# Performance work log

Measured on AMD Instinct MI355X. Metric: run time of the kernel, lower is better.

Reference implementation:

```python
import jax, jax.numpy as jnp
import numpy as np

DIMS = 3; B = 256; N = 256; K = 16; HID = 64; INC = 64; F = 64; EPG = 8192; DEPTH = 3
EPS = 1e-15


def setup_inputs() -> dict:
    key = jax.random.key(0)
    ks = jax.random.split(key, 16)
    E = B * EPG
    g = jnp.repeat(jnp.arange(B), EPG)
    row = (g * N + jax.random.randint(ks[0], (E,), 0, N)).astype(jnp.int32)
    col = (g * N + jax.random.randint(ks[1], (E,), 0, N)).astype(jnp.int32)
    edge_index = jnp.stack([row, col])
    edge_attr = jax.random.uniform(ks[2], (E, DIMS), dtype=jnp.float32)
    x = jax.random.normal(ks[3], (B * N, INC), dtype=jnp.float32)
    x_to_pool = jax.random.normal(ks[4], (B * N, F * DIMS), dtype=jnp.float32)
    batch = jnp.repeat(jnp.arange(B), N).astype(jnp.int32)
    def w(k, shape, fan):
        return (jax.random.normal(k, shape, dtype=jnp.float32) / np.float32(np.sqrt(fan)))
    return dict(
        x=x, edge_attr=edge_attr, x_to_pool=x_to_pool,
        Wm0=w(ks[5], (DIMS, INC, HID), INC), Ws0=w(ks[6], (DIMS, INC, HID), INC), b0=jnp.zeros((DIMS, HID), jnp.float32),
        Wm1=w(ks[7], (DIMS, HID, HID), HID), Ws1=w(ks[8], (DIMS, HID, HID), HID), b1=jnp.zeros((DIMS, HID), jnp.float32),
        Wm2=w(ks[9], (DIMS, HID, K), HID), Ws2=w(ks[10], (DIMS, HID, K), HID), b2=jnp.zeros((DIMS, K), jnp.float32),
        fcW1=w(ks[11], (HID * (DEPTH - 1) + K, 50), HID * (DEPTH - 1) + K), fcb1=jnp.zeros((50,), jnp.float32),
        fcW2=w(ks[12], (50, K), 50), fcb2=jnp.zeros((K,), jnp.float32),
        edge_index=edge_index, batch=batch,
    )


def reference(x, edge_attr, x_to_pool, Wm0, Ws0, b0, Wm1, Ws1, b1, Wm2, Ws2, b2,
              fcW1, fcb1, fcW2, fcb2, edge_index, batch):
    row, col = edge_index[0], edge_index[1]
    n_total = B * N

    # ---- batch_to_adj: scatter edge list into dense (dims, B, N, N) adjacency ----
    ge, rl, cl = row // N, row % N, col % N
    adj = jnp.zeros((DIMS, B, N, N), x.dtype).at[:, ge, rl, cl].add(edge_attr.T)

    # ---- ParallelResGraphConv: per-dim edge-weighted graph conv stack ----
    def gconv(h, we, Wm, Ws, b):
        agg = jax.ops.segment_sum(we[:, None] * h[col], row, num_segments=n_total)
        return jax.nn.relu(agg @ Wm + h @ Ws + b)

    assignments = []
    for d in range(DIMS):  # small fixed loop over parallel streams
        we = edge_attr[:, d]
        h0 = gconv(x, we, Wm0[d], Ws0[d], b0[d])
        h1 = gconv(h0, we, Wm1[d], Ws1[d], b1[d])
        h2 = gconv(h1, we, Wm2[d], Ws2[d], b2[d])
        conv_out = jnp.concatenate([h0, h1, h2], axis=-1)  # [BN, HID*2+K]
        logits = (conv_out @ fcW1 + fcb1) @ fcW2 + fcb2     # shared pool_fc
        assignments.append(logits)
    s = jax.nn.softmax(jnp.stack(assignments).reshape(DIMS, B, N, K), axis=-1)

    # ---- losses: modularity (edge gather) + entropy ----
    a_flat = s.reshape(DIMS, n_total, K)
    mod = jnp.float32(0.0)
    for d in range(DIMS):
        diff = a_flat[d, row] - a_flat[d, col]
        mod = mod + jnp.mean(edge_attr[:, d] * jnp.sum(diff * diff, axis=-1))
    ent = jnp.mean(jnp.sum(-s * jnp.log(s + EPS), axis=-1))
    loss = mod + ent

    # ---- DiffPool-style pooling ----
    xr = x_to_pool.reshape(n_total, F, DIMS)
    xr = jnp.transpose(xr, (2, 0, 1)).reshape(DIMS, B, N, F)
    px = jnp.einsum('dbnk,dbnf->dbkf', s, xr)
    tmp = jnp.einsum('dbnk,dbnm->dbkm', s, adj)
    padj = jnp.einsum('dbkm,dbml->dbkl', tmp, s)
    scale = jnp.float32(K / N)
    px = jnp.transpose(px, (1, 2, 3, 0)).reshape(B * K, F, DIMS) * scale
    padj = padj * (scale * scale)

    # ---- adj_to_tg_batch: dense pooled adjacency back to edge list (fixed shapes) ----
    rows = jnp.repeat(jnp.arange(K), K)
    cols = jnp.tile(jnp.arange(K), K)
    off = (jnp.arange(B) * K)[:, None]
    pei = jnp.stack([(off + rows[None, :]).reshape(-1), (off + cols[None, :]).reshape(-1)]).astype(jnp.int32)
    pea = jax.lax.stop_gradient(jnp.transpose(padj, (1, 2, 3, 0)).reshape(-1, DIMS))  # detach_pool=True
    pbatch = jnp.repeat(jnp.arange(B), K).astype(jnp.int32)
    return (px, pei, pea, pbatch, loss, s)
```

## Files before the change

### kernel.cpp

```cpp
#include <hip/hip_runtime.h>

#define DIMS 3
#define NB 256
#define NN 256
#define KK 16
#define HID 64
#define EPG 8192
#define NTOT (NB*NN)
#define NE (NB*EPG)

#define PX_OFF   0
#define PEI_OFF  786432
#define PEA_OFF  917504
#define PB_OFF   1114112
#define LOSS_OFF 1118208
#define S_OFF    1118209

#define WREC_WS  0
#define CLREC_WS 25165824
#define IPTR_WS  27262976
#define ENT_WS   27526144
#define MOD_WS   27529216
#define WC_WS    27532288
#define BC_WS    27541504

__global__ void fc_combine(const float* __restrict__ fcW1, const float* __restrict__ fcb1,
                           const float* __restrict__ fcW2, const float* __restrict__ fcb2,
                           float* __restrict__ wc, float* __restrict__ bc)
{
    const int t = threadIdx.x;
    for (int idx = t; idx < 144 * 16; idx += 256) {
        const int i = idx >> 4, k = idx & 15;
        float s = 0.f;
        for (int q = 0; q < 50; ++q) s += fcW1[i * 50 + q] * fcW2[q * 16 + k];
        wc[idx] = s;
    }
    if (t < 16) {
        float s = fcb2[t];
        for (int q = 0; q < 50; ++q) s += fcb1[q] * fcW2[q * 16 + t];
        bc[t] = s;
    }
}

#define HSTR 132
#define PSTR 129
__launch_bounds__(256)
__global__ void csr_build(const int* __restrict__ edge_index,
                          const float* __restrict__ edge_attr,
                          float* __restrict__ wrec, unsigned char* __restrict__ clrec,
                          int* __restrict__ indptr)
{
    __shared__ unsigned char  h[256 * HSTR];
    __shared__ unsigned short po[256 * PSTR];
    __shared__ int sc[256];
    const int b = blockIdx.x;
    const int t = threadIdx.x;
    const int* rowp = edge_index + (size_t)b * EPG;
    const int* colp = edge_index + (size_t)NB * EPG + (size_t)b * EPG;

    for (int i = t; i < 256 * HSTR / 4; i += 256) ((unsigned int*)h)[i] = 0u;
    __syncthreads();

    if (t < 128) {
        #pragma unroll 4
        for (int j = 0; j < 64; ++j) {
            const int r = rowp[t + 128 * j] & (NN - 1);
            h[r * HSTR + t]++;
        }
    }
    __syncthreads();

    int tot;
    {
        int s = 0;
        const unsigned int* hr = (const unsigned int*)(h + t * HSTR);
        #pragma unroll
        for (int c4 = 0; c4 < HSTR / 4; ++c4) {
            const unsigned int v = hr[c4];
            s += (v & 255) + ((v >> 8) & 255) + ((v >> 16) & 255) + (v >> 24);
        }
        tot = s;
        sc[t] = s;
    }
    __syncthreads();
    for (int ofs = 1; ofs < 256; ofs <<= 1) {
        int v = (t >= ofs) ? sc[t - ofs] : 0;
        __syncthreads();
        sc[t] += v;
        __syncthreads();
    }
    const int start = sc[t] - tot;
    indptr[b * 257 + t] = start;
    if (t == 255) indptr[b * 257 + 256] = EPG;

    {
        int run = start;
        #pragma unroll 4
        for (int c = 0; c < 128; ++c) {
            po[t * PSTR + c] = (unsigned short)run;
            run += h[t * HSTR + c];
        }
    }
    __syncthreads();

    if (t < 128) {
        const float* eap = edge_attr + (size_t)b * EPG * 3;
        float* w0 = wrec + (size_t)b * EPG;
        float* w1 = wrec + (size_t)NB * EPG + (size_t)b * EPG;
        float* w2 = wrec + 2 * (size_t)NB * EPG + (size_t)b * EPG;
        unsigned char* cdst = clrec + (size_t)b * EPG;
        #pragma unroll 2
        for (int j = 0; j < 64; ++j) {
            const int e = t + 128 * j;
            const int r = rowp[e] & (NN - 1);
            const int cl = colp[e] & (NN - 1);
            const int dest = po[r * PSTR + t]++;
            w0[dest] = eap[e * 3 + 0];
            w1[dest] = eap[e * 3 + 1];
            w2[dest] = eap[e * 3 + 2];
            cdst[dest] = (unsigned char)cl;
        }
    }
}

template<int OUTW, bool WRITE_H>
__device__ __forceinline__ void layer_step(
    int t, int r, int q, int js, int je,
    const float* __restrict__ wp, const unsigned char* __restrict__ clp,
    const float* __restrict__ Wm, const float* __restrict__ Ws,
    const float* __restrict__ bias, const float* __restrict__ wc,
    float4* hb4, float* wlds, float* lgl)
{
    constexpr int NCOL = OUTW / 4;
    constexpr int NF4  = 64 * OUTW / 4;
    {
        const float4* wmv = (const float4*)Wm;
        const float4* wsv = (const float4*)Ws;
        float4* dm = (float4*)wlds;
        float4* ds = dm + NF4;
        for (int i = t; i < NF4; i += 1024) dm[i] = wmv[i];
        for (int i = t; i < NF4; i += 1024) ds[i] = wsv[i];
    }
    __syncthreads();
    float ga[16];
    #pragma unroll
    for (int u = 0; u < 16; ++u) ga[u] = 0.f;
    const int cb = q * 4;
    for (int j = js; j < je; ++j) {
        const int cl = clp[j];
        const float w = wp[j];
        const int base = cl * 16, sw = cl & 15;
        #pragma unroll
        for (int u = 0; u < 4; ++u) {
            const float4 h4 = hb4[base + ((cb + u) ^ sw)];
            ga[u*4+0] += w * h4.x; ga[u*4+1] += w * h4.y;
            ga[u*4+2] += w * h4.z; ga[u*4+3] += w * h4.w;
        }
    }
    const int j0 = q * NCOL;
    float acc[NCOL];
    {
        const float4* bv = (const float4*)(bias + j0);
        #pragma unroll
        for (int q4 = 0; q4 < NCOL / 4; ++q4) {
            const float4 b4 = bv[q4];
            acc[q4*4+0] = b4.x; acc[q4*4+1] = b4.y; acc[q4*4+2] = b4.z; acc[q4*4+3] = b4.w;
        }
    }
    const int rbase = r * 16, rsw = r & 15;
    const float* wsl = wlds + 64 * OUTW;
    for (int ic = 0; ic < 16; ++ic) {
        const float4 h4 = hb4[rbase + (ic ^ rsw)];
        const float hv[4] = {h4.x, h4.y, h4.z, h4.w};
        #pragma unroll
        for (int u = 0; u < 4; ++u) {
            const int i = ic * 4 + u;
            const float h = hv[u];
            const float* wr = wsl + i * OUTW + j0;
            #pragma unroll
            for (int q4 = 0; q4 < NCOL / 4; ++q4) {
                const float4 w4 = *(const float4*)(wr + q4 * 4);
                acc[q4*4+0] += h * w4.x; acc[q4*4+1] += h * w4.y;
                acc[q4*4+2] += h * w4.z; acc[q4*4+3] += h * w4.w;
            }
        }
    }
    __syncthreads();
    {
        #pragma unroll
        for (int u = 0; u < 4; ++u) {
            float4 v; v.x = ga[u*4+0]; v.y = ga[u*4+1]; v.z = ga[u*4+2]; v.w = ga[u*4+3];
            hb4[rbase + ((cb + u) ^ rsw)] = v;
        }
    }
    __syncthreads();
    for (int ic = 0; ic < 16; ++ic) {
        const float4 a4 = hb4[rbase + (ic ^ rsw)];
        const float av[4] = {a4.x, a4.y, a4.z, a4.w};
        #pragma unroll
        for (int u = 0; u < 4; ++u) {
            const int i = ic * 4 + u;
            const float a = av[u];
            const float* wr = wlds + i * OUTW + j0;
            #pragma unroll
            for (int q4 = 0; q4 < NCOL / 4; ++q4) {
                const float4 w4 = *(const float4*)(wr + q4 * 4);
                acc[q4*4+0] += a * w4.x; acc[q4*4+1] += a * w4.y;
                acc[q4*4+2] += a * w4.z; acc[q4*4+3] += a * w4.w;
            }
        }
    }
    #pragma unroll
    for (int jj = 0; jj < NCOL; ++jj) acc[jj] = fmaxf(acc[jj], 0.f);
    __syncthreads();
    if (WRITE_H) {
        #pragma unroll
        for (int u = 0; u < NCOL / 4; ++u) {
            float4 v; v.x = acc[u*4+0]; v.y = acc[u*4+1]; v.z = acc[u*4+2]; v.w = acc[u*4+3];
            hb4[rbase + ((cb + u) ^ rsw)] = v;
        }
    }
    {
        float p[16];
        #pragma unroll
        for (int k = 0; k < 16; ++k) p[k] = 0.f;
        #pragma unroll
        for (int jj = 0; jj < NCOL; ++jj) {
            const float a = acc[jj];
            const float* wr = wc + (j0 + jj) * 16;
            #pragma unroll
            for (int q4 = 0; q4 < 4; ++q4) {
                const float4 w4 = *(const float4*)(wr + q4 * 4);
                p[q4*4+0] += a * w4.x; p[q4*4+1] += a * w4.y;
                p[q4*4+2] += a * w4.z; p[q4*4+3] += a * w4.w;
            }
        }
        #pragma unroll
        for (int k = 0; k < 16; ++k) p[k] += __shfl_xor(p[k], 1);
        #pragma unroll
        for (int k = 0; k < 16; ++k) p[k] += __shfl_xor(p[k], 2);
        if (q == 0) {
            float* Lr = lgl + r * 17;
            #pragma unroll
            for (int k = 0; k < 16; ++k) Lr[k] += p[k];
        }
    }
    __syncthreads();
}

__launch_bounds__(1024)
__global__ void gconv_kernel(
    const float* __restrict__ x,
    const float* __restrict__ Wm0, const float* __restrict__ Ws0, const float* __restrict__ b0,
    const float* __restrict__ Wm1, const float* __restrict__ Ws1, const float* __restrict__ b1,
    const float* __restrict__ Wm2, const float* __restrict__ Ws2, const float* __restrict__ b2,
    const float* __restrict__ wcomb, const float* __restrict__ bcomb,
    const float* __restrict__ wrec, const unsigned char* __restrict__ clrec,
    const int* __restrict__ indptr,
    float* __restrict__ out, float* __restrict__ entpart)
{
    __shared__ float4 hb4[4096];
    __shared__ float  wlds[2*64*64];
    __shared__ float  lgl[NN * 17];
    __shared__ float  red[16];
    const int t = threadIdx.x;
    const int bid = blockIdx.x;
    const int d = bid >> 8;
    const int b = bid & (NB - 1);
    const int r = t >> 2;
    const int q = t & 3;
    const int lane = t & 63;
    const int wave = t >> 6;

    {
        const float4* xv = (const float4*)(x + (size_t)b * NN * HID);
        #pragma unroll
        for (int it = 0; it < 4; ++it) {
            const int idx = t + it * 1024;
            const int nrow = idx >> 4, c = idx & 15;
            hb4[nrow * 16 + (c ^ (nrow & 15))] = xv[idx];
        }
        for (int i = t; i < NN * 17; i += 1024) lgl[i] = 0.f;
    }

    const float* wp = wrec + (size_t)d * NB * EPG + (size_t)b * EPG;
    const unsigned char* clp = clrec + (size_t)b * EPG;
    const int js = indptr[b * 257 + r];
    const int je = indptr[b * 257 + r + 1];

    layer_step<64, true >(t, r, q, js, je, wp, clp, Wm0 + d*HID*HID, Ws0 + d*HID*HID,
                          b0 + d*HID, wcomb,            hb4, wlds, lgl);
    layer_step<64, true >(t, r, q, js, je, wp, clp, Wm1 + d*HID*HID, Ws1 + d*HID*HID,
                          b1 + d*HID, wcomb + 64*16,    hb4, wlds, lgl);
    layer_step<16, false>(t, r, q, js, je, wp, clp, Wm2 + d*HID*KK,  Ws2 + d*HID*KK,
                          b2 + d*KK,  wcomb + 128*16,   hb4, wlds, lgl);

    float ent_local = 0.f;
    if (t < 256) {
        const int rr = t;
        float logits[KK];
        const float* Lr = lgl + rr * 17;
        #pragma unroll
        for (int k = 0; k < KK; ++k) logits[k] = Lr[k] + bcomb[k];
        float m = logits[0];
        #pragma unroll
        for (int k = 1; k < KK; ++k) m = fmaxf(m, logits[k]);
        float sum = 0.f, sv[KK];
        #pragma unroll
        for (int k = 0; k < KK; ++k) { sv[k] = expf(logits[k] - m); sum += sv[k]; }
        const float inv = 1.f / sum;
        float4* sp4 = (float4*)(out + S_OFF + ((size_t)(d * NB + b) * NN + rr) * KK);
        #pragma unroll
        for (int q4 = 0; q4 < 4; ++q4) {
            float4 v;
            const float s0 = sv[q4*4+0] * inv, s1 = sv[q4*4+1] * inv;
            const float s2 = sv[q4*4+2] * inv, s3 = sv[q4*4+3] * inv;
            v.x = s0; v.y = s1; v.z = s2; v.w = s3;
            sp4[q4] = v;
            ent_local -= s0 * logf(s0 + 1e-15f) + s1 * logf(s1 + 1e-15f)
                       + s2 * logf(s2 + 1e-15f) + s3 * logf(s3 + 1e-15f);
        }
    }
    #pragma unroll
    for (int off = 32; off; off >>= 1) ent_local += __shfl_down(ent_local, off);
    if (lane == 0) red[wave] = ent_local;
    __syncthreads();
    if (t == 0) {
        float s = 0.f;
        #pragma unroll
        for (int w = 0; w < 16; ++w) s += red[w];
        entpart[bid] = s;
    }
}

#define SSTR 20
__launch_bounds__(256)
__global__ void pool_kernel(
    const float* __restrict__ x_to_pool,
    const float* __restrict__ wrec, const unsigned char* __restrict__ clrec,
    const int* __restrict__ indptr,
    const float* __restrict__ out_s, float* __restrict__ out, float* __restrict__ modpart)
{
    __shared__ float sl[NN * SSTR];
    __shared__ float gl[NN * SSTR];
    __shared__ float padjw[4 * 256];
    __shared__ float red[4];
    const int t = threadIdx.x;
    const int bid = blockIdx.x;
    const int d = bid >> 8;
    const int b = bid & (NB - 1);
    const int lane = t & 63;
    const int wave = t >> 6;

    {
        const float4* sp4 = (const float4*)(out_s + S_OFF + (size_t)(d * NB + b) * NN * KK);
        #pragma unroll
        for (int it = 0; it < 4; ++it) {
            const int idx = t + it * 256;
            const int nrow = idx >> 2, c = idx & 3;
            *(float4*)(sl + nrow * SSTR + c * 4) = sp4[idx];
        }
    }
    __syncthreads();

    const float* wp = wrec + (size_t)d * NB * EPG + (size_t)b * EPG;
    const unsigned char* clp = clrec + (size_t)b * EPG;
    const int js = indptr[b * 257 + t];
    const int je = indptr[b * 257 + t + 1];
    float sr[16];
    {
        #pragma unroll
        for (int c = 0; c < 4; ++c) {
            const float4 v = *(const float4*)(sl + t * SSTR + c * 4);
            sr[c*4+0] = v.x; sr[c*4+1] = v.y; sr[c*4+2] = v.z; sr[c*4+3] = v.w;
        }
    }
    float g[16];
    #pragma unroll
    for (int k = 0; k < 16; ++k) g[k] = 0.f;
    float modacc = 0.f;
    for (int j = js; j < je; ++j) {
        const int cl = clp[j];
        const float w = wp[j];
        const float* srow = sl + cl * SSTR;
        float ss = 0.f;
        #pragma unroll
        for (int c = 0; c < 4; ++c) {
            const float4 sv = *(const float4*)(srow + c * 4);
            g[c*4+0] += w * sv.x; g[c*4+1] += w * sv.y;
            g[c*4+2] += w * sv.z; g[c*4+3] += w * sv.w;
            const float d0 = sr[c*4+0] - sv.x, d1 = sr[c*4+1] - sv.y;
            const float d2 = sr[c*4+2] - sv.z, d3 = sr[c*4+3] - sv.w;
            ss += d0*d0 + d1*d1 + d2*d2 + d3*d3;
        }
        modacc += w * ss;
    }
    {
        #pragma unroll
        for (int c = 0; c < 4; ++c) {
            float4 v; v.x = g[c*4+0]; v.y = g[c*4+1]; v.z = g[c*4+2]; v.w = g[c*4+3];
            *(float4*)(gl + t * SSTR + c * 4) = v;
        }
    }
    __syncthreads();

    {
        const int k = t & 15, lg = (t >> 4) & 3;
        float p0 = 0.f, p1 = 0.f, p2 = 0.f, p3 = 0.f;
        const int r0 = wave * 64;
        for (int rr = r0; rr < r0 + 64; ++rr) {
            const float sk = sl[rr * SSTR + k];
            const float4 g4 = *(const float4*)(gl + rr * SSTR + lg * 4);
            p0 += sk * g4.x; p1 += sk * g4.y; p2 += sk * g4.z; p3 += sk * g4.w;
        }
        float* pw = padjw + wave * 256 + k * 16 + lg * 4;
        pw[0] = p0; pw[1] = p1; pw[2] = p2; pw[3] = p3;
    }

    {
        const int f = t & 63;
        const int kg = t >> 6;
        float xa0 = 0.f, xa1 = 0.f, xa2 = 0.f, xa3 = 0.f;
        const float* xp = x_to_pool + (size_t)b * NN * (64 * DIMS) + f * DIMS + d;
        #pragma unroll 4
        for (int nn2 = 0; nn2 < NN; ++nn2) {
            const float xv = xp[(size_t)nn2 * (64 * DIMS)];
            const float4 s4 = *(const float4*)(sl + nn2 * SSTR + kg * 4);
            xa0 += xv * s4.x; xa1 += xv * s4.y; xa2 += xv * s4.z; xa3 += xv * s4.w;
        }
        const float sc = 1.f / 16.f;
        out[PX_OFF + ((size_t)((b * KK + kg * 4 + 0) * 64) + f) * DIMS + d] = xa0 * sc;
        out[PX_OFF + ((size_t)((b * KK + kg * 4 + 1) * 64) + f) * DIMS + d] = xa1 * sc;
        out[PX_OFF + ((size_t)((b * KK + kg * 4 + 2) * 64) + f) * DIMS + d] = xa2 * sc;
        out[PX_OFF + ((size_t)((b * KK + kg * 4 + 3) * 64) + f) * DIMS + d] = xa3 * sc;
    }

    #pragma unroll
    for (int off = 32; off; off >>= 1) modacc += __shfl_down(modacc, off);
    if (lane == 0) red[wave] = modacc;
    __syncthreads();
    if (t == 0) modpart[bid] = red[0] + red[1] + red[2] + red[3];

    {
        const float v = (padjw[t] + padjw[256 + t] + padjw[512 + t] + padjw[768 + t]) * (1.f / 256.f);
        out[PEA_OFF + (size_t)((b * KK + (t >> 4)) * KK + (t & 15)) * DIMS + d] = v;
    }
}

__global__ void aux_kernel(float* __restrict__ out)
{
    const int idx = blockIdx.x * 256 + threadIdx.x;
    if (idx < 2 * NTOT) {
        const int r = idx & (NTOT - 1);
        const int bb = r >> 8;
        const int j = r & 255;
        const int v = (idx < NTOT) ? (bb * KK + (j >> 4)) : (bb * KK + (j & 15));
        out[PEI_OFF + idx] = (float)v;
    } else if (idx < 2 * NTOT + NB * KK) {
        const int i = idx - 2 * NTOT;
        out[PB_OFF + i] = (float)(i >> 4);
    }
}

__global__ void loss_kernel(const float* __restrict__ entpart,
                            const float* __restrict__ modpart,
                            float* __restrict__ out)
{
    const int tid = threadIdx.x;
    float e = 0.f, m = 0.f;
    for (int i = tid; i < DIMS * NB; i += 256) { e += entpart[i]; m += modpart[i]; }
    #pragma unroll
    for (int off = 32; off; off >>= 1) { e += __shfl_down(e, off); m += __shfl_down(m, off); }
    __shared__ float er[4], mr[4];
    const int wave = tid >> 6, lane = tid & 63;
    if (lane == 0) { er[wave] = e; mr[wave] = m; }
    __syncthreads();
    if (tid == 0) {
        const float es = er[0] + er[1] + er[2] + er[3];
        const float ms = mr[0] + mr[1] + mr[2] + mr[3];
        out[LOSS_OFF] = ms / (float)NE + es / (float)(DIMS * NTOT);
    }
}

extern "C" void kernel_launch(void* const* d_in, const int* in_sizes, int n_in,
                              void* d_out, int out_size, void* d_ws, size_t ws_size,
                              hipStream_t stream)
{
    const float* x         = (const float*)d_in[0];
    const float* edge_attr = (const float*)d_in[1];
    const float* x_to_pool = (const float*)d_in[2];
    const float* Wm0 = (const float*)d_in[3];
    const float* Ws0 = (const float*)d_in[4];
    const float* b0  = (const float*)d_in[5];
    const float* Wm1 = (const float*)d_in[6];
    const float* Ws1 = (const float*)d_in[7];
    const float* b1  = (const float*)d_in[8];
    const float* Wm2 = (const float*)d_in[9];
    const float* Ws2 = (const float*)d_in[10];
    const float* b2  = (const float*)d_in[11];
    const float* fcW1= (const float*)d_in[12];
    const float* fcb1= (const float*)d_in[13];
    const float* fcW2= (const float*)d_in[14];
    const float* fcb2= (const float*)d_in[15];
    const int* edge_index = (const int*)d_in[16];
    float* out = (float*)d_out;
    char* ws = (char*)d_ws;
    float*         wrec  = (float*)(ws + WREC_WS);
    unsigned char* clrec = (unsigned char*)(ws + CLREC_WS);
    int*           iptr  = (int*)(ws + IPTR_WS);
    float*         entpart = (float*)(ws + ENT_WS);
    float*         modpart = (float*)(ws + MOD_WS);
    float*         wc    = (float*)(ws + WC_WS);
    float*         bc    = (float*)(ws + BC_WS);

    csr_build<<<dim3(NB), dim3(256), 0, stream>>>(edge_index, edge_attr, wrec, clrec, iptr);
    fc_combine<<<dim3(1), dim3(256), 0, stream>>>(fcW1, fcb1, fcW2, fcb2, wc, bc);
    gconv_kernel<<<dim3(DIMS * NB), dim3(1024), 0, stream>>>(
        x, Wm0, Ws0, b0, Wm1, Ws1, b1, Wm2, Ws2, b2,
        wc, bc, wrec, clrec, iptr, out, entpart);
    pool_kernel<<<dim3(DIMS * NB), dim3(256), 0, stream>>>(
        x_to_pool, wrec, clrec, iptr, out, out, modpart);
    aux_kernel<<<dim3((2 * NTOT + NB * KK + 255) / 256), dim3(256), 0, stream>>>(out);
    loss_kernel<<<dim3(1), dim3(256), 0, stream>>>(entpart, modpart, out);
}
```

Before: 624.6 us.

## Process two rows per thread in gconv, read weights from global, separate aggregate buffer

The gconv kernel now runs 512 threads per block, and each thread handles two node rows, so every weight load serves two rows. Weights are read straight from global memory (through the cache) instead of being staged in LDS, and the aggregated features go into a separate LDS buffer. This allows the Wm and Ws products to be fused into one pass and removes some barriers. In exchange, each thread needs more registers, the edge loops for the two rows run serially, and the weight reads go to global or cache rather than LDS.

```diff
diff --git a/kernel.cpp b/kernel.cpp
--- a/kernel.cpp
+++ b/kernel.cpp
@@ -125,130 +125,141 @@
 
 template<int OUTW, bool WRITE_H>
 __device__ __forceinline__ void layer_step(
-    int t, int r, int q, int js, int je,
+    int rg, int q, int js0, int je0, int je1,
     const float* __restrict__ wp, const unsigned char* __restrict__ clp,
     const float* __restrict__ Wm, const float* __restrict__ Ws,
     const float* __restrict__ bias, const float* __restrict__ wc,
-    float4* hb4, float* wlds, float* lgl)
+    float4* hb4, float4* ab4, float* lgl)
 {
     constexpr int NCOL = OUTW / 4;
-    constexpr int NF4  = 64 * OUTW / 4;
-    {
-        const float4* wmv = (const float4*)Wm;
-        const float4* wsv = (const float4*)Ws;
-        float4* dm = (float4*)wlds;
-        float4* ds = dm + NF4;
-        for (int i = t; i < NF4; i += 1024) dm[i] = wmv[i];
-        for (int i = t; i < NF4; i += 1024) ds[i] = wsv[i];
-    }
-    __syncthreads();
-    float ga[16];
-    #pragma unroll
-    for (int u = 0; u < 16; ++u) ga[u] = 0.f;
+    const int r0 = rg * 2, r1 = r0 + 1;
+    const int base0 = r0 * 16, sw0 = r0 & 15;
+    const int base1 = r1 * 16, sw1 = r1 & 15;
     const int cb = q * 4;
-    for (int j = js; j < je; ++j) {
+
+    float ga0[16], ga1[16];
+    #pragma unroll
+    for (int u = 0; u < 16; ++u) { ga0[u] = 0.f; ga1[u] = 0.f; }
+    for (int j = js0; j < je0; ++j) {
         const int cl = clp[j];
         const float w = wp[j];
         const int base = cl * 16, sw = cl & 15;
         #pragma unroll
         for (int u = 0; u < 4; ++u) {
             const float4 h4 = hb4[base + ((cb + u) ^ sw)];
-            ga[u*4+0] += w * h4.x; ga[u*4+1] += w * h4.y;
-            ga[u*4+2] += w * h4.z; ga[u*4+3] += w * h4.w;
-        }
-    }
+            ga0[u*4+0] += w * h4.x; ga0[u*4+1] += w * h4.y;
+            ga0[u*4+2] += w * h4.z; ga0[u*4+3] += w * h4.w;
+        }
+    }
+    for (int j = je0; j < je1; ++j) {
+        const int cl = clp[j];
+        const float w = wp[j];
+        const int base = cl * 16, sw = cl & 15;
+        #pragma unroll
+        for (int u = 0; u < 4; ++u) {
+            const float4 h4 = hb4[base + ((cb + u) ^ sw)];
+            ga1[u*4+0] += w * h4.x; ga1[u*4+1] += w * h4.y;
+            ga1[u*4+2] += w * h4.z; ga1[u*4+3] += w * h4.w;
+        }
+    }
+    #pragma unroll
+    for (int u = 0; u < 4; ++u) {
+        float4 v0; v0.x = ga0[u*4+0]; v0.y = ga0[u*4+1]; v0.z = ga0[u*4+2]; v0.w = ga0[u*4+3];
+        ab4[base0 + ((cb + u) ^ sw0)] = v0;
+        float4 v1; v1.x = ga1[u*4+0]; v1.y = ga1[u*4+1]; v1.z = ga1[u*4+2]; v1.w = ga1[u*4+3];
+        ab4[base1 + ((cb + u) ^ sw1)] = v1;
+    }
+    __syncthreads();
+
     const int j0 = q * NCOL;
-    float acc[NCOL];
+    float acc0[NCOL], acc1[NCOL];
     {
         const float4* bv = (const float4*)(bias + j0);
         #pragma unroll
         for (int q4 = 0; q4 < NCOL / 4; ++q4) {
             const float4 b4 = bv[q4];
-            acc[q4*4+0] = b4.x; acc[q4*4+1] = b4.y; acc[q4*4+2] = b4.z; acc[q4*4+3] = b4.w;
-        }
-    }
-    const int rbase = r * 16, rsw = r & 15;
-    const float* wsl = wlds + 64 * OUTW;
+            acc0[q4*4+0] = b4.x; acc0[q4*4+1] = b4.y; acc0[q4*4+2] = b4.z; acc0[q4*4+3] = b4.w;
+            acc1[q4*4+0] = b4.x; acc1[q4*4+1] = b4.y; acc1[q4*4+2] = b4.z; acc1[q4*4+3] = b4.w;
+        }
+    }
     for (int ic = 0; ic < 16; ++ic) {
-        const float4 h4 = hb4[rbase + (ic ^ rsw)];
-        const float hv[4] = {h4.x, h4.y, h4.z, h4.w};
+        const float4 h40 = hb4[base0 + (ic ^ sw0)];
+        const float4 h41 = hb4[base1 + (ic ^ sw1)];
+        const float4 a40 = ab4[base0 + (ic ^ sw0)];
+        const float4 a41 = ab4[base1 + (ic ^ sw1)];
+        const float h0v[4] = {h40.x, h40.y, h40.z, h40.w};
+        const float h1v[4] = {h41.x, h41.y, h41.z, h41.w};
+        const float a0v[4] = {a40.x, a40.y, a40.z, a40.w};
+        const float a1v[4] = {a41.x, a41.y, a41.z, a41.w};
         #pragma unroll
         for (int u = 0; u < 4; ++u) {
             const int i = ic * 4 + u;
-            const float h = hv[u];
-            const float* wr = wsl + i * OUTW + j0;
+            const float* wmr = Wm + i * OUTW + j0;
+            const float* wsr = Ws + i * OUTW + j0;
+            const float h0 = h0v[u], h1 = h1v[u], a0 = a0v[u], a1 = a1v[u];
             #pragma unroll
             for (int q4 = 0; q4 < NCOL / 4; ++q4) {
-                const float4 w4 = *(const float4*)(wr + q4 * 4);
-                acc[q4*4+0] += h * w4.x; acc[q4*4+1] += h * w4.y;
-                acc[q4*4+2] += h * w4.z; acc[q4*4+3] += h * w4.w;
+                const float4 wm4 = *(const float4*)(wmr + q4 * 4);
+                const float4 ws4 = *(const float4*)(wsr + q4 * 4);
+                acc0[q4*4+0] += a0 * wm4.x + h0 * ws4.x;
+                acc0[q4*4+1] += a0 * wm4.y + h0 * ws4.y;
+                acc0[q4*4+2] += a0 * wm4.z + h0 * ws4.z;
+                acc0[q4*4+3] += a0 * wm4.w + h0 * ws4.w;
+                acc1[q4*4+0] += a1 * wm4.x + h1 * ws4.x;
+                acc1[q4*4+1] += a1 * wm4.y + h1 * ws4.y;
+                acc1[q4*4+2] += a1 * wm4.z + h1 * ws4.z;
+                acc1[q4*4+3] += a1 * wm4.w + h1 * ws4.w;
             }
         }
     }
-    __syncthreads();
-    {
-        #pragma unroll
-        for (int u = 0; u < 4; ++u) {
-            float4 v; v.x = ga[u*4+0]; v.y = ga[u*4+1]; v.z = ga[u*4+2]; v.w = ga[u*4+3];
-            hb4[rbase + ((cb + u) ^ rsw)] = v;
-        }
-    }
-    __syncthreads();
-    for (int ic = 0; ic < 16; ++ic) {
-        const float4 a4 = hb4[rbase + (ic ^ rsw)];
-        const float av[4] = {a4.x, a4.y, a4.z, a4.w};
-        #pragma unroll
-        for (int u = 0; u < 4; ++u) {
-            const int i = ic * 4 + u;
-            const float a = av[u];
-            const float* wr = wlds + i * OUTW + j0;
-            #pragma unroll
-            for (int q4 = 0; q4 < NCOL / 4; ++q4) {
-                const float4 w4 = *(const float4*)(wr + q4 * 4);
-                acc[q4*4+0] += a * w4.x; acc[q4*4+1] += a * w4.y;
-                acc[q4*4+2] += a * w4.z; acc[q4*4+3] += a * w4.w;
-            }
-        }
-    }
-    #pragma unroll
-    for (int jj = 0; jj < NCOL; ++jj) acc[jj] = fmaxf(acc[jj], 0.f);
-    __syncthreads();
+    #pragma unroll
+    for (int jj = 0; jj < NCOL; ++jj) {
+        acc0[jj] = fmaxf(acc0[jj], 0.f);
+        acc1[jj] = fmaxf(acc1[jj], 0.f);
+    }
+    __syncthreads();
+
     if (WRITE_H) {
         #pragma unroll
         for (int u = 0; u < NCOL / 4; ++u) {
-            float4 v; v.x = acc[u*4+0]; v.y = acc[u*4+1]; v.z = acc[u*4+2]; v.w = acc[u*4+3];
-            hb4[rbase + ((cb + u) ^ rsw)] = v;
-        }
-    }
-    {
-        float p[16];
-        #pragma unroll
-        for (int k = 0; k < 16; ++k) p[k] = 0.f;
+            float4 v0; v0.x = acc0[u*4+0]; v0.y = acc0[u*4+1]; v0.z = acc0[u*4+2]; v0.w = acc0[u*4+3];
+            hb4[base0 + ((cb + u) ^ sw0)] = v0;
+            float4 v1; v1.x = acc1[u*4+0]; v1.y = acc1[u*4+1]; v1.z = acc1[u*4+2]; v1.w = acc1[u*4+3];
+            hb4[base1 + ((cb + u) ^ sw1)] = v1;
+        }
+    }
+    {
+        float p0[16], p1[16];
+        #pragma unroll
+        for (int k = 0; k < 16; ++k) { p0[k] = 0.f; p1[k] = 0.f; }
         #pragma unroll
         for (int jj = 0; jj < NCOL; ++jj) {
-            const float a = acc[jj];
+            const float a0 = acc0[jj], a1 = acc1[jj];
             const float* wr = wc + (j0 + jj) * 16;
             #pragma unroll
             for (int q4 = 0; q4 < 4; ++q4) {
                 const float4 w4 = *(const float4*)(wr + q4 * 4);
-                p[q4*4+0] += a * w4.x; p[q4*4+1] += a * w4.y;
-                p[q4*4+2] += a * w4.z; p[q4*4+3] += a * w4.w;
+                p0[q4*4+0] += a0 * w4.x; p0[q4*4+1] += a0 * w4.y;
+                p0[q4*4+2] += a0 * w4.z; p0[q4*4+3] += a0 * w4.w;
+                p1[q4*4+0] += a1 * w4.x; p1[q4*4+1] += a1 * w4.y;
+                p1[q4*4+2] += a1 * w4.z; p1[q4*4+3] += a1 * w4.w;
             }
         }
         #pragma unroll
-        for (int k = 0; k < 16; ++k) p[k] += __shfl_xor(p[k], 1);
-        #pragma unroll
-        for (int k = 0; k < 16; ++k) p[k] += __shfl_xor(p[k], 2);
+        for (int k = 0; k < 16; ++k) { p0[k] += __shfl_xor(p0[k], 1); p1[k] += __shfl_xor(p1[k], 1); }
+        #pragma unroll
+        for (int k = 0; k < 16; ++k) { p0[k] += __shfl_xor(p0[k], 2); p1[k] += __shfl_xor(p1[k], 2); }
         if (q == 0) {
-            float* Lr = lgl + r * 17;
+            float* L0 = lgl + r0 * 17;
+            float* L1 = lgl + r1 * 17;
             #pragma unroll
-            for (int k = 0; k < 16; ++k) Lr[k] += p[k];
-        }
-    }
-    __syncthreads();
-}
-
-__launch_bounds__(1024)
+            for (int k = 0; k < 16; ++k) { L0[k] += p0[k]; L1[k] += p1[k]; }
+        }
+    }
+    __syncthreads();
+}
+
+__launch_bounds__(512)
 __global__ void gconv_kernel(
     const float* __restrict__ x,
     const float* __restrict__ Wm0, const float* __restrict__ Ws0, const float* __restrict__ b0,
@@ -260,14 +271,14 @@
     float* __restrict__ out, float* __restrict__ entpart)
 {
     __shared__ float4 hb4[4096];
-    __shared__ float  wlds[2*64*64];
+    __shared__ float4 ab4[4096];
     __shared__ float  lgl[NN * 17];
-    __shared__ float  red[16];
+    __shared__ float  red[8];
     const int t = threadIdx.x;
     const int bid = blockIdx.x;
     const int d = bid >> 8;
     const int b = bid & (NB - 1);
-    const int r = t >> 2;
+    const int rg = t >> 2;
     const int q = t & 3;
     const int lane = t & 63;
     const int wave = t >> 6;
@@ -275,25 +286,27 @@
     {
         const float4* xv = (const float4*)(x + (size_t)b * NN * HID);
         #pragma unroll
-        for (int it = 0; it < 4; ++it) {
-            const int idx = t + it * 1024;
+        for (int it = 0; it < 8; ++it) {
+            const int idx = t + it * 512;
             const int nrow = idx >> 4, c = idx & 15;
             hb4[nrow * 16 + (c ^ (nrow & 15))] = xv[idx];
         }
-        for (int i = t; i < NN * 17; i += 1024) lgl[i] = 0.f;
-    }
+        for (int i = t; i < NN * 17; i += 512) lgl[i] = 0.f;
+    }
+    __syncthreads();
 
     const float* wp = wrec + (size_t)d * NB * EPG + (size_t)b * EPG;
     const unsigned char* clp = clrec + (size_t)b * EPG;
-    const int js = indptr[b * 257 + r];
-    const int je = indptr[b * 257 + r + 1];
-
-    layer_step<64, true >(t, r, q, js, je, wp, clp, Wm0 + d*HID*HID, Ws0 + d*HID*HID,
-                          b0 + d*HID, wcomb,            hb4, wlds, lgl);
-    layer_step<64, true >(t, r, q, js, je, wp, clp, Wm1 + d*HID*HID, Ws1 + d*HID*HID,
-                          b1 + d*HID, wcomb + 64*16,    hb4, wlds, lgl);
-    layer_step<16, false>(t, r, q, js, je, wp, clp, Wm2 + d*HID*KK,  Ws2 + d*HID*KK,
-                          b2 + d*KK,  wcomb + 128*16,   hb4, wlds, lgl);
+    const int js0 = indptr[b * 257 + rg * 2];
+    const int je0 = indptr[b * 257 + rg * 2 + 1];
+    const int je1 = indptr[b * 257 + rg * 2 + 2];
+
+    layer_step<64, true >(rg, q, js0, je0, je1, wp, clp, Wm0 + d*HID*HID, Ws0 + d*HID*HID,
+                          b0 + d*HID, wcomb,            hb4, ab4, lgl);
+    layer_step<64, true >(rg, q, js0, je0, je1, wp, clp, Wm1 + d*HID*HID, Ws1 + d*HID*HID,
+                          b1 + d*HID, wcomb + 64*16,    hb4, ab4, lgl);
+    layer_step<16, false>(rg, q, js0, je0, je1, wp, clp, Wm2 + d*HID*KK,  Ws2 + d*HID*KK,
+                          b2 + d*KK,  wcomb + 128*16,   hb4, ab4, lgl);
 
     float ent_local = 0.f;
     if (t < 256) {
@@ -328,7 +341,7 @@
     if (t == 0) {
         float s = 0.f;
         #pragma unroll
-        for (int w = 0; w < 16; ++w) s += red[w];
+        for (int w = 0; w < 8; ++w) s += red[w];
         entpart[bid] = s;
     }
 }
@@ -515,7 +528,7 @@
 
     csr_build<<<dim3(NB), dim3(256), 0, stream>>>(edge_index, edge_attr, wrec, clrec, iptr);
     fc_combine<<<dim3(1), dim3(256), 0, stream>>>(fcW1, fcb1, fcW2, fcb2, wc, bc);
-    gconv_kernel<<<dim3(DIMS * NB), dim3(1024), 0, stream>>>(
+    gconv_kernel<<<dim3(DIMS * NB), dim3(512), 0, stream>>>(
         x, Wm0, Ws0, b0, Wm1, Ws1, b1, Wm2, Ws2, b2,
         wc, bc, wrec, clrec, iptr, out, entpart);
     pool_kernel<<<dim3(DIMS * NB), dim3(256), 0, stream>>>(
```

Result: slower. 807.2 us (+29.2%).

## Read layer weights from global memory and fuse the two dense matmul passes

Applied to the files above, without the earlier changes.

Stops staging Wm/Ws into shared memory and instead reads the weight rows directly from global memory, relying on the cache because every row-group reads the same addresses. The aggregated neighbour features go into a separate shared buffer, so the self and message matmuls run in one fused loop and one barrier pair per layer is removed. The logit projection now reads values back from shared memory rather than registers. The risk is higher global/L1 load pressure in the inner matmul loop, plus a doubled hb4-sized LDS footprint that may limit occupancy.

```diff
diff --git a/kernel.cpp b/kernel.cpp
--- a/kernel.cpp
+++ b/kernel.cpp
@@ -125,27 +125,19 @@
 
 template<int OUTW, bool WRITE_H>
 __device__ __forceinline__ void layer_step(
-    int t, int r, int q, int js, int je,
+    int r, int q, int js, int je,
     const float* __restrict__ wp, const unsigned char* __restrict__ clp,
     const float* __restrict__ Wm, const float* __restrict__ Ws,
     const float* __restrict__ bias, const float* __restrict__ wc,
-    float4* hb4, float* wlds, float* lgl)
+    float4* hb4, float4* ab4, float* lgl)
 {
     constexpr int NCOL = OUTW / 4;
-    constexpr int NF4  = 64 * OUTW / 4;
-    {
-        const float4* wmv = (const float4*)Wm;
-        const float4* wsv = (const float4*)Ws;
-        float4* dm = (float4*)wlds;
-        float4* ds = dm + NF4;
-        for (int i = t; i < NF4; i += 1024) dm[i] = wmv[i];
-        for (int i = t; i < NF4; i += 1024) ds[i] = wsv[i];
-    }
-    __syncthreads();
+    const int rbase = r * 16, rsw = r & 15;
+    const int cb = q * 4;
+
     float ga[16];
     #pragma unroll
     for (int u = 0; u < 16; ++u) ga[u] = 0.f;
-    const int cb = q * 4;
     for (int j = js; j < je; ++j) {
         const int cl = clp[j];
         const float w = wp[j];
@@ -157,6 +149,13 @@
             ga[u*4+2] += w * h4.z; ga[u*4+3] += w * h4.w;
         }
     }
+    #pragma unroll
+    for (int u = 0; u < 4; ++u) {
+        float4 v; v.x = ga[u*4+0]; v.y = ga[u*4+1]; v.z = ga[u*4+2]; v.w = ga[u*4+3];
+        ab4[rbase + ((cb + u) ^ rsw)] = v;
+    }
+    __syncthreads();
+
     const int j0 = q * NCOL;
     float acc[NCOL];
     {
@@ -167,72 +166,78 @@
             acc[q4*4+0] = b4.x; acc[q4*4+1] = b4.y; acc[q4*4+2] = b4.z; acc[q4*4+3] = b4.w;
         }
     }
-    const int rbase = r * 16, rsw = r & 15;
-    const float* wsl = wlds + 64 * OUTW;
     for (int ic = 0; ic < 16; ++ic) {
         const float4 h4 = hb4[rbase + (ic ^ rsw)];
+        const float4 a4 = ab4[rbase + (ic ^ rsw)];
         const float hv[4] = {h4.x, h4.y, h4.z, h4.w};
+        const float av[4] = {a4.x, a4.y, a4.z, a4.w};
         #pragma unroll
         for (int u = 0; u < 4; ++u) {
             const int i = ic * 4 + u;
-            const float h = hv[u];
-            const float* wr = wsl + i * OUTW + j0;
+            const float* wmr = Wm + i * OUTW + j0;
+            const float* wsr = Ws + i * OUTW + j0;
+            const float hh = hv[u], aa = av[u];
             #pragma unroll
             for (int q4 = 0; q4 < NCOL / 4; ++q4) {
-                const float4 w4 = *(const float4*)(wr + q4 * 4);
-                acc[q4*4+0] += h * w4.x; acc[q4*4+1] += h * w4.y;
-                acc[q4*4+2] += h * w4.z; acc[q4*4+3] += h * w4.w;
+                const float4 wm4 = *(const float4*)(wmr + q4 * 4);
+                const float4 ws4 = *(const float4*)(wsr + q4 * 4);
+                acc[q4*4+0] += aa * wm4.x + hh * ws4.x;
+                acc[q4*4+1] += aa * wm4.y + hh * ws4.y;
+                acc[q4*4+2] += aa * wm4.z + hh * ws4.z;
+                acc[q4*4+3] += aa * wm4.w + hh * ws4.w;
             }
         }
     }
-    __syncthreads();
-    {
-        #pragma unroll
-        for (int u = 0; u < 4; ++u) {
-            float4 v; v.x = ga[u*4+0]; v.y = ga[u*4+1]; v.z = ga[u*4+2]; v.w = ga[u*4+3];
-            hb4[rbase + ((cb + u) ^ rsw)] = v;
-        }
-    }
-    __syncthreads();
-    for (int ic = 0; ic < 16; ++ic) {
-        const float4 a4 = hb4[rbase + (ic ^ rsw)];
-        const float av[4] = {a4.x, a4.y, a4.z, a4.w};
-        #pragma unroll
-        for (int u = 0; u < 4; ++u) {
-            const int i = ic * 4 + u;
-            const float a = av[u];
-            const float* wr = wlds + i * OUTW + j0;
-            #pragma unroll
-            for (int q4 = 0; q4 < NCOL / 4; ++q4) {
-                const float4 w4 = *(const float4*)(wr + q4 * 4);
-                acc[q4*4+0] += a * w4.x; acc[q4*4+1] += a * w4.y;
-                acc[q4*4+2] += a * w4.z; acc[q4*4+3] += a * w4.w;
-            }
-        }
-    }
     #pragma unroll
     for (int jj = 0; jj < NCOL; ++jj) acc[jj] = fmaxf(acc[jj], 0.f);
     __syncthreads();
+
     if (WRITE_H) {
         #pragma unroll
         for (int u = 0; u < NCOL / 4; ++u) {
             float4 v; v.x = acc[u*4+0]; v.y = acc[u*4+1]; v.z = acc[u*4+2]; v.w = acc[u*4+3];
             hb4[rbase + ((cb + u) ^ rsw)] = v;
         }
-    }
+    } else {
+        float4 v; v.x = acc[0]; v.y = acc[1]; v.z = acc[2]; v.w = acc[3];
+        ab4[rbase + (q ^ rsw)] = v;
+    }
+    __syncthreads();
+
     {
         float p[16];
         #pragma unroll
         for (int k = 0; k < 16; ++k) p[k] = 0.f;
-        #pragma unroll
-        for (int jj = 0; jj < NCOL; ++jj) {
-            const float a = acc[jj];
-            const float* wr = wc + (j0 + jj) * 16;
+        if (WRITE_H) {
             #pragma unroll
-            for (int q4 = 0; q4 < 4; ++q4) {
-                const float4 w4 = *(const float4*)(wr + q4 * 4);
-                p[q4*4+0] += a * w4.x; p[q4*4+1] += a * w4.y;
-                p[q4*4+2] += a * w4.z; p[q4*4+3] += a * w4.w;
+            for (int u = 0; u < 4; ++u) {
+                const float4 v4 = hb4[rbase + ((cb + u) ^ rsw)];
+                const float vv[4] = {v4.x, v4.y, v4.z, v4.w};
+                #pragma unroll
+                for (int e = 0; e < 4; ++e) {
+                    const float a = vv[e];
+                    const float* wr = wc + (j0 + u * 4 + e) * 16;
+                    #pragma unroll
+                    for (int q4 = 0; q4 < 4; ++q4) {
+                        const float4 w4 = *(const float4*)(wr + q4 * 4);
+                        p[q4*4+0] += a * w4.x; p[q4*4+1] += a * w4.y;
+                        p[q4*4+2] += a * w4.z; p[q4*4+3] += a * w4.w;
+                    }
+                }
+            }
+        } else {
+            const float4 v4 = ab4[rbase + (q ^ rsw)];
+            const float vv[4] = {v4.x, v4.y, v4.z, v4.w};
+            #pragma unroll
+            for (int e = 0; e < 4; ++e) {
+                const float a = vv[e];
+                const float* wr = wc + (j0 + e) * 16;
+                #pragma unroll
+                for (int q4 = 0; q4 < 4; ++q4) {
+                    const float4 w4 = *(const float4*)(wr + q4 * 4);
+                    p[q4*4+0] += a * w4.x; p[q4*4+1] += a * w4.y;
+                    p[q4*4+2] += a * w4.z; p[q4*4+3] += a * w4.w;
+                }
             }
         }
         #pragma unroll
@@ -245,7 +250,6 @@
             for (int k = 0; k < 16; ++k) Lr[k] += p[k];
         }
     }
-    __syncthreads();
 }
 
 __launch_bounds__(1024)
@@ -260,7 +264,7 @@
     float* __restrict__ out, float* __restrict__ entpart)
 {
     __shared__ float4 hb4[4096];
-    __shared__ float  wlds[2*64*64];
+    __shared__ float4 ab4[4096];
     __shared__ float  lgl[NN * 17];
     __shared__ float  red[16];
     const int t = threadIdx.x;
@@ -282,18 +286,20 @@
         }
         for (int i = t; i < NN * 17; i += 1024) lgl[i] = 0.f;
     }
+    __syncthreads();
 
     const float* wp = wrec + (size_t)d * NB * EPG + (size_t)b * EPG;
     const unsigned char* clp = clrec + (size_t)b * EPG;
     const int js = indptr[b * 257 + r];
     const int je = indptr[b * 257 + r + 1];
 
-    layer_step<64, true >(t, r, q, js, je, wp, clp, Wm0 + d*HID*HID, Ws0 + d*HID*HID,
-                          b0 + d*HID, wcomb,            hb4, wlds, lgl);
-    layer_step<64, true >(t, r, q, js, je, wp, clp, Wm1 + d*HID*HID, Ws1 + d*HID*HID,
-                          b1 + d*HID, wcomb + 64*16,    hb4, wlds, lgl);
-    layer_step<16, false>(t, r, q, js, je, wp, clp, Wm2 + d*HID*KK,  Ws2 + d*HID*KK,
-                          b2 + d*KK,  wcomb + 128*16,   hb4, wlds, lgl);
+    layer_step<64, true >(r, q, js, je, wp, clp, Wm0 + d*HID*HID, Ws0 + d*HID*HID,
+                          b0 + d*HID, wcomb,            hb4, ab4, lgl);
+    layer_step<64, true >(r, q, js, je, wp, clp, Wm1 + d*HID*HID, Ws1 + d*HID*HID,
+                          b1 + d*HID, wcomb + 64*16,    hb4, ab4, lgl);
+    layer_step<16, false>(r, q, js, je, wp, clp, Wm2 + d*HID*KK,  Ws2 + d*HID*KK,
+                          b2 + d*KK,  wcomb + 128*16,   hb4, ab4, lgl);
+    __syncthreads();
 
     float ent_local = 0.f;
     if (t < 256) {
```

New measurement: 1.248 ms. +99.8%, slower.
